# Kernel tuning notes

Measured on AMD Instinct MI355X. Metric: run time of the kernel, lower is better.

Reference implementation:

```python
import jax, jax.numpy as jnp
import numpy as np

N_HEADS = 8


def setup_inputs() -> dict:
    key = jax.random.key(0)
    qkv = jax.random.normal(key, (4, 1536, 2048), dtype=jnp.float32)
    return {"qkv": qkv}


def reference(qkv):
    bs, width, length = qkv.shape
    assert width % (3 * N_HEADS) == 0
    ch = width // (3 * N_HEADS)
    q, k, v = jnp.split(qkv, 3, axis=1)            # each [bs, H*C, T]
    scale = 1.0 / (ch ** 0.25)                      # 1/sqrt(sqrt(ch)) applied to both q and k
    q = (q * scale).reshape(bs * N_HEADS, ch, length)
    k = (k * scale).reshape(bs * N_HEADS, ch, length)
    v = v.reshape(bs * N_HEADS, ch, length)
    weight = jnp.einsum('bct,bcs->bts', q, k)       # [bs*H, T, T]
    weight = jax.nn.softmax(weight.astype(jnp.float32), axis=-1).astype(weight.dtype)
    a = jnp.einsum('bts,bcs->bct', weight, v)       # [bs*H, C, T]
    return a.reshape(bs, -1, length)
```

## Files before the change

### kernel.cpp

```cpp
#include <hip/hip_runtime.h>


typedef _Float16 half8  __attribute__((ext_vector_type(8)));
typedef _Float16 half4  __attribute__((ext_vector_type(4)));
typedef __fp16   fp16x2 __attribute__((ext_vector_type(2)));
typedef float    floatx4 __attribute__((ext_vector_type(4)));

constexpr int T    = 2048;
constexpr int TQ   = 128;
constexpr int TS   = 64;
constexpr int LROW = 64;
constexpr int KHALF  = TS * LROW;
constexpr int SMEM_H = 9216;
constexpr int NIT  = T / TS;
constexpr float QSCALE = 0.125f * 1.44269504088896340736f;

union h4u { half4 v; fp16x2 h2[2]; };
union h8u { half8 v; fp16x2 h2[4]; };

__device__ __forceinline__ half4 pack4(float a, float b, float c, float d) {
    h4u u;
    u.h2[0] = __builtin_amdgcn_cvt_pkrtz(a, b);
    u.h2[1] = __builtin_amdgcn_cvt_pkrtz(c, d);
    return u.v;
}

__global__ __launch_bounds__(512, 4)
void qkv_attn_kernel(const float* __restrict__ qkv, float* __restrict__ out) {
    __shared__ __align__(16) _Float16 smem[2][SMEM_H];

    const int tid  = threadIdx.x;
    const int wave = tid >> 6;
    const int lane = tid & 63;
    const int n16  = lane & 15;
    const int g    = lane >> 4;
    const int h    = wave >> 2;
    const int qg   = wave & 3;

    const int bx = blockIdx.x;
    const int hd = bx & 31;
    const int qt = bx >> 5;
    const int b  = hd >> 3;
    const int hh = hd & 7;
    const int q0 = qt * TQ;

    const float* __restrict__ qbase = qkv + (size_t)(b * 1536 + hh * 64) * T;
    const float* __restrict__ kbase = qkv + (size_t)(b * 1536 + 512 + hh * 64) * T;
    const float* __restrict__ vbase = qkv + (size_t)(b * 1536 + 1024 + hh * 64) * T;
    float* __restrict__ obase = out + (size_t)(b * 512 + hh * 64) * T;

    const bool kstage = (wave < 4);
    const int ptid = tid & 255;
    const int ks   = ((ptid >> 6) << 4) | (ptid & 15);
    const int kc4  = ((ptid >> 4) & 3) << 2;
    const int vc   = ptid >> 4;
    const int vt   = ptid & 15;
    const int vcol = 32 * (vt >> 3) + 8 * (vt & 3) + 4 * ((vt >> 2) & 1);

    int koff[4];
#pragma unroll
    for (int i = 0; i < 4; ++i) koff[i] = (i * 16 + kc4) ^ ((ks & 7) << 3);
    const int vco = vcol ^ ((vc & 7) << 3);
    const int nswz = (n16 & 7) << 3;
    const int kcolA = (g * 8) ^ nswz;
    const int kcolB = (32 + g * 8) ^ nswz;
    const int vcolr = (h * 32 + g * 8) ^ nswz;

    float pre[16];
    auto prefetch = [&](int s0) {
        if (kstage) {
            const float* kg = kbase + s0 + ks;
#pragma unroll
            for (int i = 0; i < 4; ++i) {
                const int c = i * 16 + kc4;
#pragma unroll
                for (int j = 0; j < 4; ++j) pre[i * 4 + j] = kg[(c + j) * T];
            }
        } else {
            const float* vg = vbase + vc * T + s0 + vt * 4;
#pragma unroll
            for (int i = 0; i < 4; ++i) {
                const floatx4 vv = *(const floatx4*)&vg[i * 16 * T];
                pre[i * 4 + 0] = vv.x; pre[i * 4 + 1] = vv.y;
                pre[i * 4 + 2] = vv.z; pre[i * 4 + 3] = vv.w;
            }
        }
    };
    auto flush = [&](int buf) {
        if (kstage) {
            _Float16* kd = &smem[buf][ks * LROW];
#pragma unroll
            for (int i = 0; i < 4; ++i)
                *(half4*)&kd[koff[i]] =
                    pack4(pre[i * 4], pre[i * 4 + 1], pre[i * 4 + 2], pre[i * 4 + 3]);
        } else {
            _Float16* vd = &smem[buf][KHALF + vc * LROW + vco];
#pragma unroll
            for (int i = 0; i < 4; ++i)
                *(half4*)&vd[i * 16 * LROW] =
                    pack4(pre[i * 4], pre[i * 4 + 1], pre[i * 4 + 2], pre[i * 4 + 3]);
        }
    };

    half8 bq[2][2];
    floatx4 oacc[4][2];
    floatx4 lacc[2];
    half8 aone;
#pragma unroll
    for (int i = 0; i < 8; ++i) aone[i] = (_Float16)1.f;

#pragma unroll
    for (int qt2 = 0; qt2 < 2; ++qt2) {
        const int q = q0 + qg * 32 + qt2 * 16 + n16;
#pragma unroll
        for (int kcA = 0; kcA < 2; ++kcA)
#pragma unroll
            for (int j = 0; j < 8; ++j) {
                const int c = kcA * 32 + g * 8 + j;
                bq[qt2][kcA][j] = (_Float16)(qbase[c * T + q] * QSCALE);
            }
    }
#pragma unroll
    for (int mt = 0; mt < 4; ++mt)
#pragma unroll
        for (int qt2 = 0; qt2 < 2; ++qt2) oacc[mt][qt2] = (floatx4)(0.f);
    lacc[0] = (floatx4)(0.f);
    lacc[1] = (floatx4)(0.f);

    prefetch(0);
    flush(0);
    __syncthreads();

    for (int it = 0; it < NIT; ++it) {
        const int buf = it & 1;
        if (it + 1 < NIT) prefetch((it + 1) * TS);

        const _Float16* kb = &smem[buf][0];
        const _Float16* vb = &smem[buf][KHALF];

        half8 av[4];
#pragma unroll
        for (int mt = 0; mt < 4; ++mt)
            av[mt] = *(const half8*)&vb[(mt * 16 + n16) * LROW + vcolr];

        floatx4 sacc[2][2];
#pragma unroll
        for (int sub = 0; sub < 2; ++sub) {
            const int srow = (h * 2 + sub) * 16 + n16;
            const half8 ak0 = *(const half8*)&kb[srow * LROW + kcolA];
            const half8 ak1 = *(const half8*)&kb[srow * LROW + kcolB];
            __builtin_amdgcn_s_setprio(1);
#pragma unroll
            for (int qt2 = 0; qt2 < 2; ++qt2) {
                floatx4 acc = (floatx4)(0.f);
                acc = __builtin_amdgcn_mfma_f32_16x16x32_f16(ak0, bq[qt2][0], acc, 0, 0, 0);
                acc = __builtin_amdgcn_mfma_f32_16x16x32_f16(ak1, bq[qt2][1], acc, 0, 0, 0);
                sacc[qt2][sub] = acc;
            }
            __builtin_amdgcn_s_setprio(0);
        }

#pragma unroll
        for (int qt2 = 0; qt2 < 2; ++qt2) {
            h8u bp;
#pragma unroll
            for (int i = 0; i < 4; ++i) {
                const float e0 = __builtin_amdgcn_exp2f(sacc[qt2][i >> 1][(i & 1) * 2 + 0]);
                const float e1 = __builtin_amdgcn_exp2f(sacc[qt2][i >> 1][(i & 1) * 2 + 1]);
                bp.h2[i] = __builtin_amdgcn_cvt_pkrtz(e0, e1);
            }
            __builtin_amdgcn_s_setprio(1);
#pragma unroll
            for (int mt = 0; mt < 4; ++mt)
                oacc[mt][qt2] = __builtin_amdgcn_mfma_f32_16x16x32_f16(
                    av[mt], bp.v, oacc[mt][qt2], 0, 0, 0);
            lacc[qt2] = __builtin_amdgcn_mfma_f32_16x16x32_f16(
                aone, bp.v, lacc[qt2], 0, 0, 0);
            __builtin_amdgcn_s_setprio(0);
        }

        if (it + 1 < NIT) flush(buf ^ 1);
        __syncthreads();
    }

    float* red = (float*)&smem[0][0];
    const int rbase = (qg * 64 + lane) * 36;
    if (h == 1) {
#pragma unroll
        for (int qt2 = 0; qt2 < 2; ++qt2)
#pragma unroll
            for (int mt = 0; mt < 4; ++mt)
                *(floatx4*)&red[rbase + (qt2 * 4 + mt) * 4] = oacc[mt][qt2];
        red[rbase + 32] = lacc[0][0];
        red[rbase + 33] = lacc[1][0];
    }
    __syncthreads();
    if (h == 0) {
#pragma unroll
        for (int qt2 = 0; qt2 < 2; ++qt2)
#pragma unroll
            for (int mt = 0; mt < 4; ++mt)
                oacc[mt][qt2] += *(const floatx4*)&red[rbase + (qt2 * 4 + mt) * 4];
#pragma unroll
        for (int qt2 = 0; qt2 < 2; ++qt2) {
            const float l = lacc[qt2][0] + red[rbase + 32 + qt2];
            const float linv = 1.0f / l;
            const int tcol = q0 + qg * 32 + qt2 * 16 + n16;
#pragma unroll
            for (int mt = 0; mt < 4; ++mt)
#pragma unroll
                for (int r = 0; r < 4; ++r)
                    obase[(mt * 16 + g * 4 + r) * T + tcol] = oacc[mt][qt2][r] * linv;
        }
    }
}

extern "C" void kernel_launch(void* const* d_in, const int* in_sizes, int n_in,
                              void* d_out, int out_size, void* d_ws, size_t ws_size,
                              hipStream_t stream) {
    const float* qkv = (const float*)d_in[0];
    float* out = (float*)d_out;
    qkv_attn_kernel<<<dim3(512), dim3(512), 0, stream>>>(qkv, out);
}
```

Measured before the change: 121.7 us.

## Software-pipeline QK^T and softmax-PV across iterations, replace ones-MFMA row sum

The main loop is restructured into a two-stage software pipeline. Each iteration computes the S=QK^T MFMAs for the current tile while running exp2 and the PV MFMAs for the previous tile, with ping-pong register sets and a peeled first and last iteration. The row-sum MFMA against a ones vector is replaced by scalar float accumulation of the exponentials, reduced with cross-lane shuffles at the end. This cuts MFMA count and lets exp work overlap matrix work, at the cost of more live registers, which risks spills or lower occupancy under the 512x4 launch bounds.

```diff
diff --git a/kernel.cpp b/kernel.cpp
--- a/kernel.cpp
+++ b/kernel.cpp
@@ -104,10 +104,7 @@
 
     half8 bq[2][2];
     floatx4 oacc[4][2];
-    floatx4 lacc[2];
-    half8 aone;
-#pragma unroll
-    for (int i = 0; i < 8; ++i) aone[i] = (_Float16)1.f;
+    float lsum[2];
 
 #pragma unroll
     for (int qt2 = 0; qt2 < 2; ++qt2) {
@@ -124,64 +121,84 @@
     for (int mt = 0; mt < 4; ++mt)
 #pragma unroll
         for (int qt2 = 0; qt2 < 2; ++qt2) oacc[mt][qt2] = (floatx4)(0.f);
-    lacc[0] = (floatx4)(0.f);
-    lacc[1] = (floatx4)(0.f);
+    lsum[0] = 0.f; lsum[1] = 0.f;
+
+    floatx4 sA[2][2], sB[2][2];
+    half8   aA[4],   aB[4];
+
+    auto smpv = [&](floatx4 (&sP)[2][2], half8 (&aP)[4]) {
+#pragma unroll
+        for (int qt2 = 0; qt2 < 2; ++qt2) {
+            h8u bp;
+            float ls = 0.f;
+#pragma unroll
+            for (int i = 0; i < 4; ++i) {
+                const float e0 = __builtin_amdgcn_exp2f(sP[qt2][i >> 1][(i & 1) * 2 + 0]);
+                const float e1 = __builtin_amdgcn_exp2f(sP[qt2][i >> 1][(i & 1) * 2 + 1]);
+                ls += e0 + e1;
+                bp.h2[i] = __builtin_amdgcn_cvt_pkrtz(e0, e1);
+            }
+            lsum[qt2] += ls;
+            __builtin_amdgcn_s_setprio(1);
+#pragma unroll
+            for (int mt = 0; mt < 4; ++mt)
+                oacc[mt][qt2] = __builtin_amdgcn_mfma_f32_16x16x32_f16(
+                    aP[mt], bp.v, oacc[mt][qt2], 0, 0, 0);
+            __builtin_amdgcn_s_setprio(0);
+        }
+    };
+
+    auto body = [&](floatx4 (&sP)[2][2], half8 (&aP)[4],
+                    floatx4 (&sC)[2][2], half8 (&aC)[4],
+                    int it, bool first, bool last) {
+        const int buf = it & 1;
+        if (!last) prefetch((it + 1) * TS);
+
+        const _Float16* kb = &smem[buf][0];
+        const _Float16* vb = &smem[buf][KHALF];
+
+        half8 ak0[2], ak1[2];
+#pragma unroll
+        for (int sub = 0; sub < 2; ++sub) {
+            const int srow = (h * 2 + sub) * 16 + n16;
+            ak0[sub] = *(const half8*)&kb[srow * LROW + kcolA];
+            ak1[sub] = *(const half8*)&kb[srow * LROW + kcolB];
+        }
+
+        if (!first) smpv(sP, aP);
+
+#pragma unroll
+        for (int sub = 0; sub < 2; ++sub) {
+            __builtin_amdgcn_s_setprio(1);
+#pragma unroll
+            for (int qt2 = 0; qt2 < 2; ++qt2) {
+                floatx4 acc = (floatx4)(0.f);
+                acc = __builtin_amdgcn_mfma_f32_16x16x32_f16(ak0[sub], bq[qt2][0], acc, 0, 0, 0);
+                acc = __builtin_amdgcn_mfma_f32_16x16x32_f16(ak1[sub], bq[qt2][1], acc, 0, 0, 0);
+                sC[qt2][sub] = acc;
+            }
+            __builtin_amdgcn_s_setprio(0);
+        }
+
+#pragma unroll
+        for (int mt = 0; mt < 4; ++mt)
+            aC[mt] = *(const half8*)&vb[(mt * 16 + n16) * LROW + vcolr];
+
+        if (!last) flush(buf ^ 1);
+        __syncthreads();
+    };
 
     prefetch(0);
     flush(0);
     __syncthreads();
 
-    for (int it = 0; it < NIT; ++it) {
-        const int buf = it & 1;
-        if (it + 1 < NIT) prefetch((it + 1) * TS);
-
-        const _Float16* kb = &smem[buf][0];
-        const _Float16* vb = &smem[buf][KHALF];
-
-        half8 av[4];
-#pragma unroll
-        for (int mt = 0; mt < 4; ++mt)
-            av[mt] = *(const half8*)&vb[(mt * 16 + n16) * LROW + vcolr];
-
-        floatx4 sacc[2][2];
-#pragma unroll
-        for (int sub = 0; sub < 2; ++sub) {
-            const int srow = (h * 2 + sub) * 16 + n16;
-            const half8 ak0 = *(const half8*)&kb[srow * LROW + kcolA];
-            const half8 ak1 = *(const half8*)&kb[srow * LROW + kcolB];
-            __builtin_amdgcn_s_setprio(1);
-#pragma unroll
-            for (int qt2 = 0; qt2 < 2; ++qt2) {
-                floatx4 acc = (floatx4)(0.f);
-                acc = __builtin_amdgcn_mfma_f32_16x16x32_f16(ak0, bq[qt2][0], acc, 0, 0, 0);
-                acc = __builtin_amdgcn_mfma_f32_16x16x32_f16(ak1, bq[qt2][1], acc, 0, 0, 0);
-                sacc[qt2][sub] = acc;
-            }
-            __builtin_amdgcn_s_setprio(0);
-        }
-
-#pragma unroll
-        for (int qt2 = 0; qt2 < 2; ++qt2) {
-            h8u bp;
-#pragma unroll
-            for (int i = 0; i < 4; ++i) {
-                const float e0 = __builtin_amdgcn_exp2f(sacc[qt2][i >> 1][(i & 1) * 2 + 0]);
-                const float e1 = __builtin_amdgcn_exp2f(sacc[qt2][i >> 1][(i & 1) * 2 + 1]);
-                bp.h2[i] = __builtin_amdgcn_cvt_pkrtz(e0, e1);
-            }
-            __builtin_amdgcn_s_setprio(1);
-#pragma unroll
-            for (int mt = 0; mt < 4; ++mt)
-                oacc[mt][qt2] = __builtin_amdgcn_mfma_f32_16x16x32_f16(
-                    av[mt], bp.v, oacc[mt][qt2], 0, 0, 0);
-            lacc[qt2] = __builtin_amdgcn_mfma_f32_16x16x32_f16(
-                aone, bp.v, lacc[qt2], 0, 0, 0);
-            __builtin_amdgcn_s_setprio(0);
-        }
-
-        if (it + 1 < NIT) flush(buf ^ 1);
-        __syncthreads();
-    }
+    body(sA, aA, sA, aA, 0, true, false);
+    for (int it = 1; it + 1 < NIT; it += 2) {
+        body(sA, aA, sB, aB, it, false, false);
+        body(sB, aB, sA, aA, it + 1, false, false);
+    }
+    body(sA, aA, sB, aB, NIT - 1, false, true);
+    smpv(sB, aB);
 
     float* red = (float*)&smem[0][0];
     const int rbase = (qg * 64 + lane) * 36;
@@ -191,8 +208,8 @@
 #pragma unroll
             for (int mt = 0; mt < 4; ++mt)
                 *(floatx4*)&red[rbase + (qt2 * 4 + mt) * 4] = oacc[mt][qt2];
-        red[rbase + 32] = lacc[0][0];
-        red[rbase + 33] = lacc[1][0];
+        red[rbase + 32] = lsum[0];
+        red[rbase + 33] = lsum[1];
     }
     __syncthreads();
     if (h == 0) {
@@ -201,9 +218,13 @@
 #pragma unroll
             for (int mt = 0; mt < 4; ++mt)
                 oacc[mt][qt2] += *(const floatx4*)&red[rbase + (qt2 * 4 + mt) * 4];
+        lsum[0] += red[rbase + 32];
+        lsum[1] += red[rbase + 33];
 #pragma unroll
         for (int qt2 = 0; qt2 < 2; ++qt2) {
-            const float l = lacc[qt2][0] + red[rbase + 32 + qt2];
+            float l = lsum[qt2];
+            l += __shfl_xor(l, 16);
+            l += __shfl_xor(l, 32);
             const float linv = 1.0f / l;
             const int tcol = q0 + qg * 32 + qt2 * 16 + n16;
 #pragma unroll
```

Measured after the change: 267.7 us. +120.0%, slower.
